# Optimization experiments

Measured on AMD Instinct MI355X. Metric: run time of the kernel, lower is better.

The kernel has to match this reference:

```python
import jax, jax.numpy as jnp
import numpy as np

N = 4096        # nodes
F_IN = 3000     # gene/feature dim
H1, C1 = 4, 64  # conv1 heads, per-head channels -> 256 hidden
HID = H1 * C1   # 256
E = 65536       # edges (avg degree 16)
POOL_H = 128


def _gat(x, W, a_src, a_dst, bias, src, dst, ew, heads, out_ch, n):
    """GATConv: linear proj, per-edge LeakyReLU attention, segment softmax over
    destination nodes (edge_weight folded in multiplicatively), scatter-add."""
    h = (x @ W).reshape(n, heads, out_ch)            # [N,H,C]
    hs, hd = h[src], h[dst]                          # gather [E,H,C]
    e = jax.nn.leaky_relu((hs * a_src).sum(-1) + (hd * a_dst).sum(-1), 0.2)  # [E,H]
    m = jax.ops.segment_max(e, dst, num_segments=n)  # stable softmax per dst
    ex = jnp.exp(e - m[dst]) * ew[:, None]
    denom = jax.ops.segment_sum(ex, dst, num_segments=n)
    alpha = ex / (denom[dst] + 1e-16)                # [E,H]
    out = jax.ops.segment_sum(hs * alpha[..., None], dst, num_segments=n)
    return out.reshape(n, heads * out_ch) + bias


def _att_pool(emb, mask, w1, b1, w2, b2):
    scores = (jax.nn.relu(emb @ w1 + b1) @ w2 + b2)[:, 0]      # [N]
    masked = jnp.where(mask, scores[None, :], -1e9)            # broadcast to [N,N]
    wts = jax.nn.softmax(masked, axis=-1)                      # [N,N]
    g = wts @ emb                                              # [N,C]
    g = g / jnp.maximum(jnp.linalg.norm(g, axis=1, keepdims=True), 1e-12)
    return jax.nn.sigmoid(g)


def _disc(c, h_pl, h_mi, W, bb, bias):
    sc1 = jnp.einsum('nc,kcd,nd->nk', h_pl, W, c) + bb
    sc2 = jnp.einsum('nc,kcd,nd->nk', h_mi, W, c) + bb
    return jnp.concatenate([sc1, sc2], axis=1) + bias


def setup_inputs() -> dict:
    key = jax.random.key(0)
    ks = jax.random.split(key, 20)
    s = 0.05
    return {
        'feat':   jax.random.normal(ks[0], (N, F_IN), jnp.float32),
        'feat_a': jax.random.normal(ks[1], (N, F_IN), jnp.float32),
        'edge_index': jax.random.randint(ks[2], (2, E), 0, N),
        'edge_weight': jax.random.uniform(ks[3], (E,), jnp.float32),
        'graph_neigh': jax.random.randint(ks[4], (N, N), 0, 2).astype(jnp.int32),
        'W1': jax.random.normal(ks[5], (F_IN, HID), jnp.float32) * s,
        'a_src1': jax.random.normal(ks[6], (H1, C1), jnp.float32) * s,
        'a_dst1': jax.random.normal(ks[7], (H1, C1), jnp.float32) * s,
        'b1': jnp.zeros((HID,), jnp.float32),
        'W2': jax.random.normal(ks[8], (HID, F_IN), jnp.float32) * s,
        'a_src2': jax.random.normal(ks[9], (1, F_IN), jnp.float32) * s,
        'a_dst2': jax.random.normal(ks[10], (1, F_IN), jnp.float32) * s,
        'b2': jnp.zeros((F_IN,), jnp.float32),
        'pa_w1': jax.random.normal(ks[11], (HID, POOL_H), jnp.float32) * s,
        'pa_b1': jnp.zeros((POOL_H,), jnp.float32),
        'pa_w2': jax.random.normal(ks[12], (POOL_H, 1), jnp.float32) * s,
        'pa_b2': jnp.zeros((1,), jnp.float32),
        'disc_w': jax.random.normal(ks[13], (1, HID, HID), jnp.float32) * s,
        'disc_bb': jnp.zeros((1,), jnp.float32),
        'disc_bias': jnp.zeros((1,), jnp.float32),
    }


def reference(feat, feat_a, edge_index, edge_weight, graph_neigh,
              W1, a_src1, a_dst1, b1, W2, a_src2, a_dst2, b2,
              pa_w1, pa_b1, pa_w2, pa_b2, disc_w, disc_bb, disc_bias):
    src, dst = edge_index[0], edge_index[1]
    mask = graph_neigh.astype(bool)
    # branch 1 (dropout=0, eval mode)
    z = jax.nn.relu(_gat(feat, W1, a_src1, a_dst1, b1, src, dst, edge_weight, H1, C1, N))
    hidden_emb = z
    h = _gat(z, W2, a_src2, a_dst2, b2, src, dst, edge_weight, 1, F_IN, N)
    emb = jax.nn.relu(z)  # == z (relu idempotent)
    # augmented branch
    z_a = jax.nn.relu(_gat(feat_a, W1, a_src1, a_dst1, b1, src, dst, edge_weight, H1, C1, N))
    emb_a = jax.nn.relu(z_a)
    # attention pooling + sigmoid (shared params for both calls; original
    # re-initializes a random pooling per call, which is not deterministic)
    g = _att_pool(emb, mask, pa_w1, pa_b1, pa_w2, pa_b2)
    g_a = _att_pool(emb_a, mask, pa_w1, pa_b1, pa_w2, pa_b2)
    ret = _disc(g, emb, emb_a, disc_w, disc_bb, disc_bias)
    ret_a = _disc(g_a, emb_a, emb, disc_w, disc_bb, disc_bias)
    return hidden_emb, h, ret, ret_a
```

## Files before the change

### kernel.cpp

```cpp
#include <hip/hip_runtime.h>
#include <cstdint>
#include <cstddef>

#define N_NODES 4096
#define F_INF   3000
#define FPAD    3008
#define NPAD    3072
#define HIDC    256
#define NEDGE   65536
#define POOLH   128
#define GCOLS   576

typedef unsigned short u16;
typedef __attribute__((ext_vector_type(8))) short bf16x8;
typedef __attribute__((ext_vector_type(8))) unsigned short us8;
typedef __attribute__((ext_vector_type(4))) unsigned int u32x4;
typedef __attribute__((ext_vector_type(4))) float f32x4;

__device__ inline float lrelu(float x){ return x > 0.f ? x : 0.2f*x; }
__device__ inline u16 f2b(float f){
  uint32_t x = __builtin_bit_cast(uint32_t, f);
  uint32_t r = (x + 0x7fffu + ((x >> 16) & 1u)) >> 16;
  return (u16)r;
}
__device__ inline float b2f(u16 u){
  uint32_t x = ((uint32_t)u) << 16;
  return __builtin_bit_cast(float, x);
}
__device__ __forceinline__ uint32_t cvt2(float lo, float hi){
  uint32_t r;
  asm("v_cvt_pk_bf16_f32 %0, %1, %2" : "=v"(r) : "v"(lo), "v"(hi));
  return r;
}
__device__ __forceinline__ void lds16(const void* g, void* l){
  __builtin_amdgcn_global_load_lds((const __attribute__((address_space(1))) void*)g,
                                   (__attribute__((address_space(3))) void*)l, 16, 0, 0);
}

__global__ void k_deg(const int* __restrict__ dst, int* __restrict__ deg){
  int e = blockIdx.x*256 + threadIdx.x;
  if (e < NEDGE) atomicAdd(&deg[dst[e]], 1);
}

__global__ void k_scan(const int* __restrict__ deg, int* __restrict__ off){
  __shared__ int sm[1024];
  int tid = threadIdx.x;
  int v0=deg[tid*4], v1=deg[tid*4+1], v2=deg[tid*4+2], v3=deg[tid*4+3];
  int s = v0+v1+v2+v3;
  sm[tid]=s; __syncthreads();
  for (int d=1; d<1024; d<<=1){
    int t = (tid>=d)? sm[tid-d] : 0;
    __syncthreads();
    sm[tid] += t;
    __syncthreads();
  }
  int run = sm[tid]-s;
  off[tid*4+0]=run; run+=v0;
  off[tid*4+1]=run; run+=v1;
  off[tid*4+2]=run; run+=v2;
  off[tid*4+3]=run; run+=v3;
  if (tid==1023) off[N_NODES]=run;
}

__global__ void k_fill(const int* __restrict__ ei, const float* __restrict__ ew,
                       const int* __restrict__ off, int* __restrict__ cursor,
                       int* __restrict__ csr_src, float* __restrict__ csr_w){
  int e = blockIdx.x*256+threadIdx.x;
  if (e >= NEDGE) return;
  int d = ei[NEDGE + e];
  int slot = off[d] + atomicAdd(&cursor[d],1);
  csr_src[slot] = ei[e];
  csr_w[slot] = ew[e];
}

__global__ void k_cvt(const float* __restrict__ in, u16* __restrict__ out,
                      int R, int Cin, int Cout){
  size_t i = ((size_t)blockIdx.x*256 + threadIdx.x)*4;
  if (i >= (size_t)R*Cout) return;
  int r = (int)(i / Cout), c = (int)(i % Cout);
  ushort4 o;
  if (c + 3 < Cin){
    float4 v = *(const float4*)(in + (size_t)r*Cin + c);
    o.x=f2b(v.x); o.y=f2b(v.y); o.z=f2b(v.z); o.w=f2b(v.w);
  } else {
    float vs[4];
    #pragma unroll
    for (int j=0;j<4;j++) vs[j] = (c+j<Cin)? in[(size_t)r*Cin+c+j] : 0.f;
    o.x=f2b(vs[0]); o.y=f2b(vs[1]); o.z=f2b(vs[2]); o.w=f2b(vs[3]);
  }
  *(ushort4*)(out+i) = o;
}

__global__ void k_trcvt(const float* __restrict__ in, u16* __restrict__ out,
                        int R, int C, int OCols, const float* __restrict__ scale){
  __shared__ float t[32][33];
  int c0 = blockIdx.x*32, r0 = blockIdx.y*32;
  int tx = threadIdx.x & 31, ty = threadIdx.x >> 5;
  #pragma unroll
  for (int i=0;i<4;i++){
    int r = r0 + ty + i*8, c = c0 + tx;
    float v = (r<R && c<C) ? in[(size_t)r*C + c] : 0.f;
    if (scale && r<R) v *= scale[r];
    t[ty+i*8][tx] = v;
  }
  __syncthreads();
  #pragma unroll
  for (int i=0;i<4;i++){
    int c = c0 + ty + i*8, r = r0 + tx;
    out[(size_t)c*OCols + r] = f2b(t[tx][ty+i*8]);
  }
}

template<int ATYPE, int BN, int NWM, int NWN>
__global__ __launch_bounds__(NWM*NWN*64) void k_mg(
    const void* __restrict__ A0v, const void* __restrict__ A1v, int srow,
    const u16* __restrict__ B, float* __restrict__ Cv,
    const float* __restrict__ bias,
    int M, int nmax, int K, int Ksrc,
    int lda, int ldb, int ldc, int kcount){
  constexpr int THREADS = NWM*NWN*64;
  constexpr int WM = 64/NWM, WN = BN/NWN, MR = WM/16, NR = WN/16;
  constexpr int APT = 1024/THREADS;
  constexpr int BPT = BN*8/THREADS;
  constexpr int LPT = APT + BPT;
  __shared__ __align__(16) char L[32768 + BN*256];
  const int tid = threadIdx.x;
  const int bm = blockIdx.x*64, bn = blockIdx.y*BN;
  const int lane = tid & 63, w = tid >> 6;
  const int wr = w / NWN, wc = w % NWN;
  f32x4 acc[MR][NR] = {};

  const int kbeg = blockIdx.z * kcount;
  const int kend = min(K, kbeg + kcount);
  const int nsteps = (kend - kbeg) >> 6;

  auto stage = [&](int kk, int half){
    char* bufA = L + half*16384;
    #pragma unroll
    for (int p=0;p<APT;p++){
      int s = p*THREADS + tid, row = s>>4, c = s&15, cg = c ^ (row&15);
      int gk = kk + cg*4;
      if (gk + 4 > Ksrc) gk = 0;
      int grow = bm + row;
      const char* Ap = (grow < srow)
          ? (const char*)A0v + ((size_t)grow*lda + gk)*4
          : (const char*)A1v + ((size_t)(grow-srow)*lda + gk)*4;
      lds16(Ap, bufA + (size_t)s*16);
    }
    char* bufB = L + 32768 + half*(BN*128);
    #pragma unroll
    for (int p=0;p<BPT;p++){
      int s = p*THREADS + tid, row = s>>3, c = s&7, cg = c ^ (row&7);
      lds16(B + (size_t)(bn+row)*ldb + kk + cg*8, bufB + (size_t)s*16);
    }
  };

  auto compute = [&](int half){
    char* bufA = L + half*16384;
    char* bufB = L + 32768 + half*(BN*128);
    #pragma unroll
    for (int ks=0; ks<2; ks++){
      bf16x8 af[MR], bfv[NR];
      #pragma unroll
      for (int m=0;m<MR;m++){
        int row = wr*WM + m*16 + (lane&15);
        int g = ks*8 + (lane>>4)*2;
        int x = row & 15;
        f32x4 a0 = *(const f32x4*)(bufA + row*256 + (((g  )^x)<<4));
        f32x4 a1 = *(const f32x4*)(bufA + row*256 + (((g+1)^x)<<4));
        u32x4 o;
        if (ATYPE==0){
          o[0]=cvt2(a0[0],a0[1]); o[1]=cvt2(a0[2],a0[3]);
          o[2]=cvt2(a1[0],a1[1]); o[3]=cvt2(a1[2],a1[3]);
        } else {
          u32x4 ia = __builtin_bit_cast(u32x4, a0);
          u32x4 ib = __builtin_bit_cast(u32x4, a1);
          o[0] = ia[0]*0x3F80u + ia[1]*0x3F800000u;
          o[1] = ia[2]*0x3F80u + ia[3]*0x3F800000u;
          o[2] = ib[0]*0x3F80u + ib[1]*0x3F800000u;
          o[3] = ib[2]*0x3F80u + ib[3]*0x3F800000u;
        }
        af[m] = __builtin_bit_cast(bf16x8, o);
      }
      #pragma unroll
      for (int n=0;n<NR;n++){
        int row = wc*WN + n*16 + (lane&15);
        int g = ks*4 + (lane>>4);
        bfv[n] = *(const bf16x8*)(bufB + row*128 + ((g ^ (row&7))<<4));
      }
      #pragma unroll
      for (int m=0;m<MR;m++)
        #pragma unroll
        for (int n=0;n<NR;n++)
          acc[m][n] = __builtin_amdgcn_mfma_f32_16x16x32_bf16(af[m], bfv[n], acc[m][n], 0,0,0);
    }
  };

  stage(kbeg, 0);
  if (nsteps > 1) stage(kbeg + 64, 1);

  for (int t=0; t<nsteps; ++t){
    if (t+1 < nsteps){
      if constexpr (LPT == 6) asm volatile("s_waitcnt vmcnt(6)" ::: "memory");
      else if constexpr (LPT == 5) asm volatile("s_waitcnt vmcnt(5)" ::: "memory");
      else asm volatile("s_waitcnt vmcnt(0)" ::: "memory");
    } else {
      asm volatile("s_waitcnt vmcnt(0)" ::: "memory");
    }
    __builtin_amdgcn_s_barrier();
    __builtin_amdgcn_sched_barrier(0);
    compute(t & 1);
    __builtin_amdgcn_s_barrier();
    if (t+2 < nsteps) stage(kbeg + (t+2)*64, t & 1);
  }

  const size_t slab = (size_t)blockIdx.z * (size_t)M * ldc;
  float* C = Cv + slab;
  const int rbase = bm + wr*WM + ((lane>>4)<<2);
  const int cbase = bn + wc*WN + (lane&15);
  #pragma unroll
  for (int n=0;n<NR;n++){
    int gcol = cbase + n*16;
    if (gcol >= nmax) continue;
    float bv = bias ? bias[gcol] : 0.f;
    #pragma unroll
    for (int m=0;m<MR;m++)
      #pragma unroll
      for (int j=0;j<4;j++)
        C[(size_t)(rbase + m*16 + j)*ldc + gcol] = acc[m][n][j] + bv;
  }
}

__global__ void k_hred(const float* __restrict__ S, float* __restrict__ h,
                       const float* __restrict__ a_src, const float* __restrict__ a_dst,
                       float* __restrict__ ss, float* __restrict__ sd){
  const size_t SLP = (size_t)2*N_NODES*HIDC;
  int n = blockIdx.x, c = threadIdx.x;
  size_t i = (size_t)n*HIDC + c;
  float v = S[i] + S[i+SLP];
  h[i] = v;
  float vs = v*a_src[c], vd = v*a_dst[c];
  #pragma unroll
  for (int o=32;o>0;o>>=1){ vs += __shfl_down(vs,o); vd += __shfl_down(vd,o); }
  if ((c&63)==0){ int hh=c>>6; ss[n*4+hh]=vs; sd[n*4+hh]=vd; }
}

__global__ void k_wvec(const float* __restrict__ W2, const float* __restrict__ a2s,
                       const float* __restrict__ a2d, float* __restrict__ wsrc,
                       float* __restrict__ wdst){
  __shared__ float sm[8];
  int c = blockIdx.x, t = threadIdx.x;
  const float* row = W2 + (size_t)c*F_INF;
  float vs=0.f, vd=0.f;
  for (int f=t; f<F_INF; f+=256){ float v=row[f]; vs+=v*a2s[f]; vd+=v*a2d[f]; }
  #pragma unroll
  for (int o=32;o>0;o>>=1){ vs+=__shfl_down(vs,o); vd+=__shfl_down(vd,o); }
  int lane=t&63, w=t>>6;
  if (lane==0){ sm[w]=vs; sm[4+w]=vd; }
  __syncthreads();
  if (t==0) wsrc[c]=sm[0]+sm[1]+sm[2]+sm[3];
  if (t==1) wdst[c]=sm[4]+sm[5]+sm[6]+sm[7];
}

__global__ void k_gat1(const float* __restrict__ h1st, const float* __restrict__ s_src,
                       const float* __restrict__ s_dst, const int* __restrict__ off,
                       const int* __restrict__ csr_src, const float* __restrict__ csr_w,
                       const float* __restrict__ b1, float* __restrict__ z,
                       float* __restrict__ za, const float* __restrict__ wsrc,
                       const float* __restrict__ wdst, float* __restrict__ ssz,
                       float* __restrict__ sdz){
  __shared__ int   sidx[256];
  __shared__ float scw[256];
  __shared__ float sev[256*4];
  __shared__ float smz[8];
  int nb = blockIdx.x, c = threadIdx.x, h = c>>6;
  int n = nb & (N_NODES-1), br = nb >> 12;
  const float* hm = h1st + (size_t)br*N_NODES*HIDC;
  const float* ssp = s_src + (size_t)br*N_NODES*4;
  const float* sdp = s_dst + (size_t)br*N_NODES*4;
  float* zp = br ? za : z;
  int o0 = off[n], o1 = off[n+1];
  int deg = o1 - o0;
  float4 sdv = *(const float4*)(sdp + (size_t)n*4);

  float m = -1e30f;
  for (int base=0; base<deg; base+=256){
    int cnt = min(256, deg-base);
    __syncthreads();
    if (c < cnt){
      int s = csr_src[o0+base+c];
      sidx[c] = s; scw[c] = csr_w[o0+base+c];
      float4 ss4 = *(const float4*)(ssp + (size_t)s*4);
      sev[c*4+0] = lrelu(ss4.x + sdv.x);
      sev[c*4+1] = lrelu(ss4.y + sdv.y);
      sev[c*4+2] = lrelu(ss4.z + sdv.z);
      sev[c*4+3] = lrelu(ss4.w + sdv.w);
    }
    __syncthreads();
    for (int t=0; t<cnt; t++) m = fmaxf(m, sev[t*4+h]);
  }

  const bool multi = deg > 256;
  float denom = 0.f, acc = 0.f;
  for (int base=0; base<deg; base+=256){
    int cnt = min(256, deg-base);
    if (multi){
      __syncthreads();
      if (c < cnt){
        int s = csr_src[o0+base+c];
        sidx[c] = s; scw[c] = csr_w[o0+base+c];
        float4 ss4 = *(const float4*)(ssp + (size_t)s*4);
        sev[c*4+0] = lrelu(ss4.x + sdv.x);
        sev[c*4+1] = lrelu(ss4.y + sdv.y);
        sev[c*4+2] = lrelu(ss4.z + sdv.z);
        sev[c*4+3] = lrelu(ss4.w + sdv.w);
      }
      __syncthreads();
    }
    int t = 0;
    for (; t+4 <= cnt; t += 4){
      int s0=sidx[t], s1=sidx[t+1], s2=sidx[t+2], s3=sidx[t+3];
      float w0 = __expf(sev[(t  )*4+h]-m)*scw[t  ];
      float w1 = __expf(sev[(t+1)*4+h]-m)*scw[t+1];
      float w2 = __expf(sev[(t+2)*4+h]-m)*scw[t+2];
      float w3 = __expf(sev[(t+3)*4+h]-m)*scw[t+3];
      float v0 = hm[(size_t)s0*HIDC+c];
      float v1 = hm[(size_t)s1*HIDC+c];
      float v2 = hm[(size_t)s2*HIDC+c];
      float v3 = hm[(size_t)s3*HIDC+c];
      denom += (w0+w1)+(w2+w3);
      acc += w0*v0 + w1*v1 + w2*v2 + w3*v3;
    }
    for (; t<cnt; ++t){
      int s0 = sidx[t];
      float w0 = __expf(sev[t*4+h]-m)*scw[t];
      denom += w0;
      acc += w0*hm[(size_t)s0*HIDC+c];
    }
  }

  float res = acc/(denom+1e-16f) + b1[c];
  float zv = fmaxf(res, 0.f);
  zp[(size_t)n*HIDC+c] = zv;
  if (br==0){
    float vs = zv*wsrc[c], vd = zv*wdst[c];
    #pragma unroll
    for (int o=32;o>0;o>>=1){ vs+=__shfl_down(vs,o); vd+=__shfl_down(vd,o); }
    int lane=c&63, w=c>>6;
    if (lane==0){ smz[w]=vs; smz[4+w]=vd; }
    __syncthreads();
    if (c==0) ssz[n]=smz[0]+smz[1]+smz[2]+smz[3];
    if (c==1) sdz[n]=smz[4]+smz[5]+smz[6]+smz[7];
  }
}

__global__ void k_gatz(const float* __restrict__ z, const float* __restrict__ ssz,
                       const float* __restrict__ sdz, const int* __restrict__ off,
                       const int* __restrict__ csr_src, const float* __restrict__ csr_w,
                       float* __restrict__ agg){
  __shared__ int   sidx[256];
  __shared__ float scw[256];
  __shared__ float sev[256];
  int n = blockIdx.x, c = threadIdx.x;
  int o0 = off[n], o1 = off[n+1];
  int deg = o1 - o0;
  float sd = sdz[n];

  float m = -1e30f;
  for (int base=0; base<deg; base+=256){
    int cnt = min(256, deg-base);
    __syncthreads();
    if (c < cnt){
      int s = csr_src[o0+base+c];
      sidx[c] = s; scw[c] = csr_w[o0+base+c];
      sev[c] = lrelu(ssz[s] + sd);
    }
    __syncthreads();
    for (int t=0; t<cnt; t++) m = fmaxf(m, sev[t]);
  }

  const bool multi = deg > 256;
  float denom = 0.f, acc = 0.f;
  for (int base=0; base<deg; base+=256){
    int cnt = min(256, deg-base);
    if (multi){
      __syncthreads();
      if (c < cnt){
        int s = csr_src[o0+base+c];
        sidx[c] = s; scw[c] = csr_w[o0+base+c];
        sev[c] = lrelu(ssz[s] + sd);
      }
      __syncthreads();
    }
    int t = 0;
    for (; t+4 <= cnt; t += 4){
      int s0=sidx[t], s1=sidx[t+1], s2=sidx[t+2], s3=sidx[t+3];
      float w0 = __expf(sev[t  ]-m)*scw[t  ];
      float w1 = __expf(sev[t+1]-m)*scw[t+1];
      float w2 = __expf(sev[t+2]-m)*scw[t+2];
      float w3 = __expf(sev[t+3]-m)*scw[t+3];
      float v0 = z[(size_t)s0*HIDC+c];
      float v1 = z[(size_t)s1*HIDC+c];
      float v2 = z[(size_t)s2*HIDC+c];
      float v3 = z[(size_t)s3*HIDC+c];
      denom += (w0+w1)+(w2+w3);
      acc += w0*v0 + w1*v1 + w2*v2 + w3*v3;
    }
    for (; t<cnt; ++t){
      int s0 = sidx[t];
      float w0 = __expf(sev[t]-m)*scw[t];
      denom += w0;
      acc += w0*z[(size_t)s0*HIDC+c];
    }
  }
  agg[(size_t)n*HIDC+c] = acc/(denom+1e-16f);
}

__global__ void k_score(const float* __restrict__ Hp, const float* __restrict__ b1,
                        const float* __restrict__ w2, const float* __restrict__ b2,
                        float* __restrict__ sc){
  int row = blockIdx.x*4 + (threadIdx.x>>6);
  int lane = threadIdx.x & 63;
  size_t base = (size_t)row*POOLH;
  float h0 = fmaxf(Hp[base+lane]    + b1[lane],    0.f);
  float h1 = fmaxf(Hp[base+lane+64] + b1[lane+64], 0.f);
  float v = h0*w2[lane] + h1*w2[lane+64];
  #pragma unroll
  for (int o=32;o>0;o>>=1) v += __shfl_down(v,o);
  if (lane==0) sc[row] = v + b2[0];
}

__global__ void k_maxred2(const float* __restrict__ s, float* __restrict__ M){
  __shared__ float sm[16];
  int tid=threadIdx.x;
  const float* sp = s + (size_t)blockIdx.x*N_NODES;
  float m=-1e30f;
  for (int i=tid;i<N_NODES;i+=1024) m=fmaxf(m,sp[i]);
  #pragma unroll
  for (int o=32;o>0;o>>=1) m=fmaxf(m,__shfl_down(m,o));
  if ((tid&63)==0) sm[tid>>6]=m;
  __syncthreads();
  if (tid==0){
    float mm=sm[0];
    for (int i=1;i<16;i++) mm=fmaxf(mm,sm[i]);
    M[blockIdx.x]=mm;
  }
}

__global__ void k_p2(const float* __restrict__ sc, const float* __restrict__ M,
                     float* __restrict__ pA, float* __restrict__ pB,
                     u16* __restrict__ qT){
  int i = blockIdx.x*256+threadIdx.x;
  float a = __expf(sc[i]-M[0]);
  float b = __expf(sc[N_NODES+i]-M[1]);
  pA[i]=a; pB[i]=b;
  qT[(size_t)512*N_NODES+i]=f2b(a);
  qT[(size_t)513*N_NODES+i]=f2b(b);
}

__global__ void k_gfin(const float* __restrict__ G, float* __restrict__ gA,
                       float* __restrict__ gB){
  __shared__ float sm[4];
  __shared__ float tot;
  const size_t SL = (size_t)N_NODES*GCOLS;
  int n=blockIdx.x, c=threadIdx.x;
  int brv = blockIdx.y;
  int co = brv ? HIDC : 0, dcol = brv ? 513 : 512;
  float* g = brv ? gB : gA;
  size_t base = (size_t)n*GCOLS;
  float gp=0.f, dn=0.f;
  #pragma unroll
  for (int s=0;s<4;s++){ gp += G[base+co+c+s*SL]; dn += G[base+dcol+s*SL]; }
  gp /= (dn + 1e-16f);
  float v = gp*gp;
  #pragma unroll
  for (int o=32;o>0;o>>=1) v+=__shfl_down(v,o);
  if ((c&63)==0) sm[c>>6]=v;
  __syncthreads();
  if (c==0) tot = sm[0]+sm[1]+sm[2]+sm[3];
  __syncthreads();
  float nrm = sqrtf(tot);
  float x = gp/fmaxf(nrm,1e-12f);
  g[(size_t)n*HIDC+c]=1.f/(1.f+__expf(-x));
}

__global__ void k_disc(const float* __restrict__ z, const float* __restrict__ za,
                       const float* __restrict__ V, const float* __restrict__ Va,
                       const float* __restrict__ bbp, const float* __restrict__ biasp,
                       float* __restrict__ ret, float* __restrict__ ret_a){
  __shared__ float sm[16];
  int n=blockIdx.x, c=threadIdx.x;
  float ez = z[(size_t)n*HIDC+c], ea = za[(size_t)n*HIDC+c];
  float v  = V[(size_t)n*HIDC+c], va = Va[(size_t)n*HIDC+c];
  float p1=ez*v, p2=ea*v, p3=ea*va, p4=ez*va;
  #pragma unroll
  for (int o=32;o>0;o>>=1){
    p1+=__shfl_down(p1,o); p2+=__shfl_down(p2,o);
    p3+=__shfl_down(p3,o); p4+=__shfl_down(p4,o);
  }
  int lane=c&63, w=c>>6;
  if (lane==0){ sm[w]=p1; sm[4+w]=p2; sm[8+w]=p3; sm[12+w]=p4; }
  __syncthreads();
  if (c==0){
    float add = bbp[0]+biasp[0];
    ret[n*2+0]   = sm[0]+sm[1]+sm[2]+sm[3]   + add;
    ret[n*2+1]   = sm[4]+sm[5]+sm[6]+sm[7]   + add;
    ret_a[n*2+0] = sm[8]+sm[9]+sm[10]+sm[11] + add;
    ret_a[n*2+1] = sm[12]+sm[13]+sm[14]+sm[15] + add;
  }
}

extern "C" void kernel_launch(void* const* d_in, const int* in_sizes, int n_in,
                              void* d_out, int out_size, void* d_ws, size_t ws_size,
                              hipStream_t stream){
  (void)in_sizes; (void)n_in; (void)out_size; (void)ws_size;
  const float* feat   = (const float*)d_in[0];
  const float* feat_a = (const float*)d_in[1];
  const int*   ei     = (const int*)d_in[2];
  const float* ew     = (const float*)d_in[3];
  const int*   mask   = (const int*)d_in[4];
  const float* W1     = (const float*)d_in[5];
  const float* a_src1 = (const float*)d_in[6];
  const float* a_dst1 = (const float*)d_in[7];
  const float* b1     = (const float*)d_in[8];
  const float* W2     = (const float*)d_in[9];
  const float* a_src2 = (const float*)d_in[10];
  const float* a_dst2 = (const float*)d_in[11];
  const float* b2     = (const float*)d_in[12];
  const float* pw1    = (const float*)d_in[13];
  const float* pb1    = (const float*)d_in[14];
  const float* pw2    = (const float*)d_in[15];
  const float* pb2    = (const float*)d_in[16];
  const float* dw     = (const float*)d_in[17];
  const float* dbb    = (const float*)d_in[18];
  const float* dbias  = (const float*)d_in[19];

  float* out  = (float*)d_out;
  float* z    = out;
  float* hout = out + (size_t)N_NODES*HIDC;
  float* ret  = hout + (size_t)N_NODES*F_INF;
  float* ret_a= ret + (size_t)N_NODES*2;

  char* cur = (char*)d_ws;
  auto alloc = [&](size_t bytes)->void*{
    void* p = cur; cur += (bytes + 255) & ~(size_t)255; return p;
  };
  void* SLB = alloc((size_t)4*N_NODES*GCOLS*4);
  u16* W1T  = (u16*)alloc((size_t)HIDC*FPAD*2);
  u16* W2T  = (u16*)alloc((size_t)NPAD*HIDC*2);
  u16* pw1T = (u16*)alloc((size_t)POOLH*HIDC*2);
  u16* qT   = (u16*)alloc((size_t)GCOLS*N_NODES*2);
  u16* dwb  = (u16*)alloc((size_t)HIDC*HIDC*2);
  float* h1st = (float*)alloc((size_t)2*N_NODES*HIDC*4);
  float* za   = (float*)alloc((size_t)N_NODES*HIDC*4);
  float* agg  = (float*)alloc((size_t)N_NODES*HIDC*4);
  float* Vst  = (float*)alloc((size_t)2*N_NODES*HIDC*4);
  float* gv   = (float*)alloc((size_t)N_NODES*HIDC*4);
  float* gva  = (float*)alloc((size_t)N_NODES*HIDC*4);
  float* ss1 = (float*)alloc((size_t)2*N_NODES*4*4);
  float* sd1 = (float*)alloc((size_t)2*N_NODES*4*4);
  float* ssz = (float*)alloc(N_NODES*4);
  float* sdz = (float*)alloc(N_NODES*4);
  float* wsrc= (float*)alloc(HIDC*4);
  float* wdst= (float*)alloc(HIDC*4);
  float* scAB = (float*)alloc((size_t)2*N_NODES*4);
  float* pvA = (float*)alloc(N_NODES*4);
  float* pvB = (float*)alloc(N_NODES*4);
  float* Mb  = (float*)alloc(256);
  int* deg    = (int*)alloc(N_NODES*4);
  int* off    = (int*)alloc((N_NODES+64)*4);
  int* cursor = (int*)alloc(N_NODES*4);
  int* csrc   = (int*)alloc(NEDGE*4);
  float* csw  = (float*)alloc(NEDGE*4);

  float* V   = Vst;
  float* Va  = Vst + (size_t)N_NODES*HIDC;

  hipMemsetAsync(deg, 0, N_NODES*sizeof(int), stream);
  hipMemsetAsync(cursor, 0, N_NODES*sizeof(int), stream);
  hipMemsetAsync(qT + (size_t)514*N_NODES, 0, (size_t)(GCOLS-514)*N_NODES*2, stream);
  k_deg<<<NEDGE/256,256,0,stream>>>(ei+NEDGE, deg);
  k_scan<<<1,1024,0,stream>>>(deg, off);
  k_fill<<<NEDGE/256,256,0,stream>>>(ei, ew, off, cursor, csrc, csw);
  k_wvec<<<HIDC,256,0,stream>>>(W2, a_src2, a_dst2, wsrc, wdst);

  k_trcvt<<<dim3(HIDC/32, FPAD/32),256,0,stream>>>(W1, W1T, F_INF, HIDC, FPAD, nullptr);
  k_trcvt<<<dim3(NPAD/32, HIDC/32),256,0,stream>>>(W2, W2T, HIDC, F_INF, HIDC, nullptr);
  k_trcvt<<<dim3(POOLH/32, HIDC/32),256,0,stream>>>(pw1, pw1T, HIDC, POOLH, HIDC, nullptr);
  k_cvt<<<HIDC*HIDC/4/256,256,0,stream>>>(dw, dwb, HIDC, HIDC, HIDC);

  k_mg<0,256,1,8><<<dim3(2*N_NODES/64, 1, 2),512,0,stream>>>(
      feat, feat_a, N_NODES, W1T, (float*)SLB, nullptr,
      2*N_NODES, HIDC, FPAD, F_INF, F_INF, FPAD, HIDC, 1536);
  k_hred<<<2*N_NODES,256,0,stream>>>((const float*)SLB, h1st, a_src1, a_dst1, ss1, sd1);

  k_gat1<<<2*N_NODES,256,0,stream>>>(h1st, ss1, sd1, off, csrc, csw, b1, z, za,
                                     wsrc, wdst, ssz, sdz);

  k_gatz<<<N_NODES,256,0,stream>>>(z, ssz, sdz, off, csrc, csw, agg);
  k_mg<0,64,2,2><<<dim3(N_NODES/64, FPAD/64, 1),256,0,stream>>>(
      agg, agg, N_NODES, W2T, hout, b2,
      N_NODES, F_INF, HIDC, HIDC, HIDC, HIDC, F_INF, HIDC);

  k_mg<0,64,2,2><<<dim3(2*N_NODES/64, POOLH/64, 1),256,0,stream>>>(
      z, za, N_NODES, pw1T, Vst, nullptr,
      2*N_NODES, POOLH, HIDC, HIDC, HIDC, HIDC, POOLH, HIDC);
  k_score<<<2*N_NODES/4,256,0,stream>>>(Vst, pb1, pw2, pb2, scAB);
  k_maxred2<<<2,1024,0,stream>>>(scAB, Mb);
  k_p2<<<N_NODES/256,256,0,stream>>>(scAB, Mb, pvA, pvB, qT);
  k_trcvt<<<dim3(HIDC/32, N_NODES/32),256,0,stream>>>(z,  qT, N_NODES, HIDC, N_NODES, pvA);
  k_trcvt<<<dim3(HIDC/32, N_NODES/32),256,0,stream>>>(za, qT + (size_t)HIDC*N_NODES, N_NODES, HIDC, N_NODES, pvB);

  k_mg<1,192,2,4><<<dim3(N_NODES/64, GCOLS/192, 4),512,0,stream>>>(
      mask, mask, 2*N_NODES, qT, (float*)SLB, nullptr,
      N_NODES, GCOLS, N_NODES, N_NODES, N_NODES, N_NODES, GCOLS, 1024);
  k_gfin<<<dim3(N_NODES,2),256,0,stream>>>((const float*)SLB, gv, gva);

  k_mg<0,64,2,2><<<dim3(2*N_NODES/64, HIDC/64, 1),256,0,stream>>>(
      gv, gva, N_NODES, dwb, Vst, nullptr,
      2*N_NODES, HIDC, HIDC, HIDC, HIDC, HIDC, HIDC, HIDC);
  k_disc<<<N_NODES,256,0,stream>>>(z, za, V, Va, dbb, dbias, ret, ret_a);
}
```

Before: 239.1 us.

## Parameterize GEMM K-tile, halve BK to 32, widen split-K, emit bf16 partials

Adds a template K-tile size (BK) to the shared GEMM kernel and switches all GEMMs from 64 to 32, which halves shared-memory use per block so more blocks can be resident. The B-tile swizzle is reworked to suit the narrower tile. The first projection GEMM goes from split-K 2 to split-K 4, and its partial sums, along with those of the pooling GEMM, are now written as bf16 instead of fp32. The reducers sum four bf16 slabs to cut partial-sum write and read traffic. The pooling GEMM also drops from 8 to 4 waves per block. Storing partials in bf16 costs accumulation precision, and the smaller K-tile means more barriers per unit of work.

Result: slower. 244.4 us (+2.2%).

```diff
diff --git a/kernel.cpp b/kernel.cpp
--- a/kernel.cpp
+++ b/kernel.cpp
@@ -16,6 +16,8 @@
 typedef __attribute__((ext_vector_type(8))) unsigned short us8;
 typedef __attribute__((ext_vector_type(4))) unsigned int u32x4;
 typedef __attribute__((ext_vector_type(4))) float f32x4;
+
+constexpr int ilog2c(int v){ return v<=1 ? 0 : 1+ilog2c(v>>1); }
 
 __device__ inline float lrelu(float x){ return x > 0.f ? x : 0.2f*x; }
 __device__ inline u16 f2b(float f){
@@ -111,19 +113,21 @@
   }
 }
 
-template<int ATYPE, int BN, int NWM, int NWN>
+template<int ATYPE, int BN, int BK, int NWM, int NWN, int CT>
 __global__ __launch_bounds__(NWM*NWN*64) void k_mg(
     const void* __restrict__ A0v, const void* __restrict__ A1v, int srow,
-    const u16* __restrict__ B, float* __restrict__ Cv,
+    const u16* __restrict__ B, void* __restrict__ Cv,
     const float* __restrict__ bias,
     int M, int nmax, int K, int Ksrc,
     int lda, int ldb, int ldc, int kcount){
   constexpr int THREADS = NWM*NWN*64;
   constexpr int WM = 64/NWM, WN = BN/NWN, MR = WM/16, NR = WN/16;
-  constexpr int APT = 1024/THREADS;
-  constexpr int BPT = BN*8/THREADS;
+  constexpr int CA = BK/4, CB = BK/8;
+  constexpr int LCA = ilog2c(CA), LCB = ilog2c(CB);
+  constexpr int APT = (64*CA)/THREADS, BPT = (BN*CB)/THREADS;
   constexpr int LPT = APT + BPT;
-  __shared__ __align__(16) char L[32768 + BN*256];
+  constexpr int ABYTES = 64*BK*4, BBYTES = BN*BK*2;
+  __shared__ __align__(16) char L[2*ABYTES + 2*BBYTES];
   const int tid = threadIdx.x;
   const int bm = blockIdx.x*64, bn = blockIdx.y*BN;
   const int lane = tid & 63, w = tid >> 6;
@@ -132,13 +136,14 @@
 
   const int kbeg = blockIdx.z * kcount;
   const int kend = min(K, kbeg + kcount);
-  const int nsteps = (kend - kbeg) >> 6;
+  const int nsteps = (kend - kbeg) / BK;
 
   auto stage = [&](int kk, int half){
-    char* bufA = L + half*16384;
+    char* bufA = L + half*ABYTES;
     #pragma unroll
     for (int p=0;p<APT;p++){
-      int s = p*THREADS + tid, row = s>>4, c = s&15, cg = c ^ (row&15);
+      int s = p*THREADS + tid, row = s>>LCA, c = s&(CA-1);
+      int cg = c ^ (row&(CA-1));
       int gk = kk + cg*4;
       if (gk + 4 > Ksrc) gk = 0;
       int grow = bm + row;
@@ -147,27 +152,28 @@
           : (const char*)A1v + ((size_t)(grow-srow)*lda + gk)*4;
       lds16(Ap, bufA + (size_t)s*16);
     }
-    char* bufB = L + 32768 + half*(BN*128);
+    char* bufB = L + 2*ABYTES + half*BBYTES;
     #pragma unroll
     for (int p=0;p<BPT;p++){
-      int s = p*THREADS + tid, row = s>>3, c = s&7, cg = c ^ (row&7);
-      lds16(B + (size_t)(bn+row)*ldb + kk + cg*8, bufB + (size_t)s*16);
+      int s = p*THREADS + tid, row = s>>LCB, c = s&(CB-1);
+      int xb = (row ^ (row>>2)) & (CB-1);
+      lds16(B + (size_t)(bn+row)*ldb + kk + ((c^xb)<<3), bufB + (size_t)s*16);
     }
   };
 
   auto compute = [&](int half){
-    char* bufA = L + half*16384;
-    char* bufB = L + 32768 + half*(BN*128);
+    char* bufA = L + half*ABYTES;
+    char* bufB = L + 2*ABYTES + half*BBYTES;
     #pragma unroll
-    for (int ks=0; ks<2; ks++){
+    for (int ks=0; ks<BK/32; ks++){
       bf16x8 af[MR], bfv[NR];
       #pragma unroll
       for (int m=0;m<MR;m++){
         int row = wr*WM + m*16 + (lane&15);
         int g = ks*8 + (lane>>4)*2;
-        int x = row & 15;
-        f32x4 a0 = *(const f32x4*)(bufA + row*256 + (((g  )^x)<<4));
-        f32x4 a1 = *(const f32x4*)(bufA + row*256 + (((g+1)^x)<<4));
+        int xa = row & (CA-1);
+        f32x4 a0 = *(const f32x4*)(bufA + row*(BK*4) + (((g  )^xa)<<4));
+        f32x4 a1 = *(const f32x4*)(bufA + row*(BK*4) + (((g+1)^xa)<<4));
         u32x4 o;
         if (ATYPE==0){
           o[0]=cvt2(a0[0],a0[1]); o[1]=cvt2(a0[2],a0[3]);
@@ -186,7 +192,8 @@
       for (int n=0;n<NR;n++){
         int row = wc*WN + n*16 + (lane&15);
         int g = ks*4 + (lane>>4);
-        bfv[n] = *(const bf16x8*)(bufB + row*128 + ((g ^ (row&7))<<4));
+        int xb = (row ^ (row>>2)) & (CB-1);
+        bfv[n] = *(const bf16x8*)(bufB + row*(BK*2) + ((g^xb)<<4));
       }
       #pragma unroll
       for (int m=0;m<MR;m++)
@@ -197,13 +204,16 @@
   };
 
   stage(kbeg, 0);
-  if (nsteps > 1) stage(kbeg + 64, 1);
+  if (nsteps > 1) stage(kbeg + BK, 1);
 
   for (int t=0; t<nsteps; ++t){
     if (t+1 < nsteps){
-      if constexpr (LPT == 6) asm volatile("s_waitcnt vmcnt(6)" ::: "memory");
+      if constexpr (LPT == 2)      asm volatile("s_waitcnt vmcnt(2)" ::: "memory");
+      else if constexpr (LPT == 3) asm volatile("s_waitcnt vmcnt(3)" ::: "memory");
+      else if constexpr (LPT == 4) asm volatile("s_waitcnt vmcnt(4)" ::: "memory");
       else if constexpr (LPT == 5) asm volatile("s_waitcnt vmcnt(5)" ::: "memory");
-      else asm volatile("s_waitcnt vmcnt(0)" ::: "memory");
+      else if constexpr (LPT == 6) asm volatile("s_waitcnt vmcnt(6)" ::: "memory");
+      else                         asm volatile("s_waitcnt vmcnt(0)" ::: "memory");
     } else {
       asm volatile("s_waitcnt vmcnt(0)" ::: "memory");
     }
@@ -211,33 +221,47 @@
     __builtin_amdgcn_sched_barrier(0);
     compute(t & 1);
     __builtin_amdgcn_s_barrier();
-    if (t+2 < nsteps) stage(kbeg + (t+2)*64, t & 1);
+    if (t+2 < nsteps) stage(kbeg + (t+2)*BK, t & 1);
   }
 
   const size_t slab = (size_t)blockIdx.z * (size_t)M * ldc;
-  float* C = Cv + slab;
   const int rbase = bm + wr*WM + ((lane>>4)<<2);
   const int cbase = bn + wc*WN + (lane&15);
-  #pragma unroll
-  for (int n=0;n<NR;n++){
-    int gcol = cbase + n*16;
-    if (gcol >= nmax) continue;
-    float bv = bias ? bias[gcol] : 0.f;
+  if constexpr (CT == 1){
+    u16* C = (u16*)Cv + slab;
     #pragma unroll
-    for (int m=0;m<MR;m++)
+    for (int n=0;n<NR;n++){
+      int gcol = cbase + n*16;
+      if (gcol >= nmax) continue;
       #pragma unroll
-      for (int j=0;j<4;j++)
-        C[(size_t)(rbase + m*16 + j)*ldc + gcol] = acc[m][n][j] + bv;
-  }
-}
-
-__global__ void k_hred(const float* __restrict__ S, float* __restrict__ h,
+      for (int m=0;m<MR;m++)
+        #pragma unroll
+        for (int j=0;j<4;j++)
+          C[(size_t)(rbase + m*16 + j)*ldc + gcol] = f2b(acc[m][n][j]);
+    }
+  } else {
+    float* C = (float*)Cv + slab;
+    #pragma unroll
+    for (int n=0;n<NR;n++){
+      int gcol = cbase + n*16;
+      if (gcol >= nmax) continue;
+      float bv = bias ? bias[gcol] : 0.f;
+      #pragma unroll
+      for (int m=0;m<MR;m++)
+        #pragma unroll
+        for (int j=0;j<4;j++)
+          C[(size_t)(rbase + m*16 + j)*ldc + gcol] = acc[m][n][j] + bv;
+    }
+  }
+}
+
+__global__ void k_hred(const u16* __restrict__ S, float* __restrict__ h,
                        const float* __restrict__ a_src, const float* __restrict__ a_dst,
                        float* __restrict__ ss, float* __restrict__ sd){
   const size_t SLP = (size_t)2*N_NODES*HIDC;
   int n = blockIdx.x, c = threadIdx.x;
   size_t i = (size_t)n*HIDC + c;
-  float v = S[i] + S[i+SLP];
+  float v = b2f(S[i]) + b2f(S[i+SLP]) + b2f(S[i+2*SLP]) + b2f(S[i+3*SLP]);
   h[i] = v;
   float vs = v*a_src[c], vd = v*a_dst[c];
   #pragma unroll
@@ -458,7 +482,7 @@
   qT[(size_t)513*N_NODES+i]=f2b(b);
 }
 
-__global__ void k_gfin(const float* __restrict__ G, float* __restrict__ gA,
+__global__ void k_gfin(const u16* __restrict__ G, float* __restrict__ gA,
                        float* __restrict__ gB){
   __shared__ float sm[4];
   __shared__ float tot;
@@ -470,7 +494,7 @@
   size_t base = (size_t)n*GCOLS;
   float gp=0.f, dn=0.f;
   #pragma unroll
-  for (int s=0;s<4;s++){ gp += G[base+co+c+s*SL]; dn += G[base+dcol+s*SL]; }
+  for (int s=0;s<4;s++){ gp += b2f(G[base+co+c+s*SL]); dn += b2f(G[base+dcol+s*SL]); }
   gp /= (dn + 1e-16f);
   float v = gp*gp;
   #pragma unroll
@@ -589,20 +613,20 @@
   k_trcvt<<<dim3(POOLH/32, HIDC/32),256,0,stream>>>(pw1, pw1T, HIDC, POOLH, HIDC, nullptr);
   k_cvt<<<HIDC*HIDC/4/256,256,0,stream>>>(dw, dwb, HIDC, HIDC, HIDC);
 
-  k_mg<0,256,1,8><<<dim3(2*N_NODES/64, 1, 2),512,0,stream>>>(
-      feat, feat_a, N_NODES, W1T, (float*)SLB, nullptr,
-      2*N_NODES, HIDC, FPAD, F_INF, F_INF, FPAD, HIDC, 1536);
-  k_hred<<<2*N_NODES,256,0,stream>>>((const float*)SLB, h1st, a_src1, a_dst1, ss1, sd1);
+  k_mg<0,256,32,2,4,1><<<dim3(2*N_NODES/64, 1, 4),512,0,stream>>>(
+      feat, feat_a, N_NODES, W1T, SLB, nullptr,
+      2*N_NODES, HIDC, FPAD, F_INF, F_INF, FPAD, HIDC, 768);
+  k_hred<<<2*N_NODES,256,0,stream>>>((const u16*)SLB, h1st, a_src1, a_dst1, ss1, sd1);
 
   k_gat1<<<2*N_NODES,256,0,stream>>>(h1st, ss1, sd1, off, csrc, csw, b1, z, za,
                                      wsrc, wdst, ssz, sdz);
 
   k_gatz<<<N_NODES,256,0,stream>>>(z, ssz, sdz, off, csrc, csw, agg);
-  k_mg<0,64,2,2><<<dim3(N_NODES/64, FPAD/64, 1),256,0,stream>>>(
+  k_mg<0,64,32,2,2,0><<<dim3(N_NODES/64, FPAD/64, 1),256,0,stream>>>(
       agg, agg, N_NODES, W2T, hout, b2,
       N_NODES, F_INF, HIDC, HIDC, HIDC, HIDC, F_INF, HIDC);
 
-  k_mg<0,64,2,2><<<dim3(2*N_NODES/64, POOLH/64, 1),256,0,stream>>>(
+  k_mg<0,64,32,2,2,0><<<dim3(2*N_NODES/64, POOLH/64, 1),256,0,stream>>>(
       z, za, N_NODES, pw1T, Vst, nullptr,
       2*N_NODES, POOLH, HIDC, HIDC, HIDC, HIDC, POOLH, HIDC);
   k_score<<<2*N_NODES/4,256,0,stream>>>(Vst, pb1, pw2, pb2, scAB);
@@ -611,12 +635,12 @@
   k_trcvt<<<dim3(HIDC/32, N_NODES/32),256,0,stream>>>(z,  qT, N_NODES, HIDC, N_NODES, pvA);
   k_trcvt<<<dim3(HIDC/32, N_NODES/32),256,0,stream>>>(za, qT + (size_t)HIDC*N_NODES, N_NODES, HIDC, N_NODES, pvB);
 
-  k_mg<1,192,2,4><<<dim3(N_NODES/64, GCOLS/192, 4),512,0,stream>>>(
-      mask, mask, 2*N_NODES, qT, (float*)SLB, nullptr,
+  k_mg<1,192,32,1,4,1><<<dim3(N_NODES/64, GCOLS/192, 4),256,0,stream>>>(
+      mask, mask, 2*N_NODES, qT, SLB, nullptr,
       N_NODES, GCOLS, N_NODES, N_NODES, N_NODES, N_NODES, GCOLS, 1024);
-  k_gfin<<<dim3(N_NODES,2),256,0,stream>>>((const float*)SLB, gv, gva);
-
-  k_mg<0,64,2,2><<<dim3(2*N_NODES/64, HIDC/64, 1),256,0,stream>>>(
+  k_gfin<<<dim3(N_NODES,2),256,0,stream>>>((const u16*)SLB, gv, gva);
+
+  k_mg<0,64,32,2,2,0><<<dim3(2*N_NODES/64, HIDC/64, 1),256,0,stream>>>(
       gv, gva, N_NODES, dwb, Vst, nullptr,
       2*N_NODES, HIDC, HIDC, HIDC, HIDC, HIDC, HIDC, HIDC);
   k_disc<<<N_NODES,256,0,stream>>>(z, za, V, Va, dbb, dbias, ret, ret_a);
```
